# Performance work log

Measured on AMD Instinct MI355X. Metric: run time of the kernel, lower is better.

Reference implementation:

```python
import jax, jax.numpy as jnp
import numpy as np

B, L, H, NH = 4, 1024, 768, 12
NE, M, P = 30, 6, 600
EMB, BS, NC = 768, 16, 97
NEG = -1e30


def setup_inputs() -> dict:
    key = jax.random.key(0)
    ks = jax.random.split(key, 9)
    sequence_output = jax.random.normal(ks[0], (B, L, H), jnp.float32)
    attention = jax.random.uniform(ks[1], (B, NH, L, L), jnp.float32)
    mention_idx = jax.random.randint(ks[2], (B, NE, M), 0, L)
    mention_mask = jnp.ones((B, NE, M), jnp.float32)
    hts = jax.random.randint(ks[3], (B, P, 2), 0, NE)
    s = 0.02
    head_W = jax.random.normal(ks[4], (EMB, 2 * H), jnp.float32) * s
    head_b = jnp.zeros((EMB,), jnp.float32)
    tail_W = jax.random.normal(ks[5], (EMB, 2 * H), jnp.float32) * s
    tail_b = jnp.zeros((EMB,), jnp.float32)
    proj_W = jax.random.normal(ks[6], (H, EMB * BS), jnp.float32) * s
    cls_W = jax.random.normal(ks[7], (NC, H), jnp.float32) * s
    cls_b = jnp.zeros((NC,), jnp.float32)
    return {
        'sequence_output': sequence_output, 'attention': attention,
        'head_W': head_W, 'head_b': head_b, 'tail_W': tail_W, 'tail_b': tail_b,
        'proj_W': proj_W, 'cls_W': cls_W, 'cls_b': cls_b,
        'mention_mask': mention_mask, 'mention_idx': mention_idx, 'hts': hts,
    }


def reference(sequence_output, attention, head_W, head_b, tail_W, tail_b,
              proj_W, cls_W, cls_b, mention_mask, mention_idx, hts):
    b_, l_, h_ = sequence_output.shape
    bidx = jnp.arange(b_)[:, None, None]                     # [B,1,1]
    # ---- per-entity pooling (segment reduce over ragged mentions) ----
    m_emb = sequence_output[bidx, mention_idx]               # [B,NE,M,H]
    att_t = attention.transpose(0, 2, 1, 3)                  # [B,L,NH,L]
    m_att = att_t[bidx, mention_idx]                         # [B,NE,M,NH,L]
    masked = jnp.where(mention_mask[..., None] > 0, m_emb, NEG)
    e_emb = jax.nn.logsumexp(masked, axis=2)                 # [B,NE,H]
    cnt = jnp.maximum(mention_mask.sum(2), 1.0)              # [B,NE]
    e_att = (m_att * mention_mask[..., None, None]).sum(2) / cnt[..., None, None]  # [B,NE,NH,L]
    # ---- head/tail gathers over pairs ----
    b2 = jnp.arange(b_)[:, None]                             # [B,1]
    h_emb = e_emb[b2, hts[..., 0]]                           # [B,P,H]
    t_emb = e_emb[b2, hts[..., 1]]
    h_att = e_att[b2, hts[..., 0]]                           # [B,P,NH,L]
    t_att = e_att[b2, hts[..., 1]]
    ht_att = (h_att * t_att).mean(2)                         # [B,P,L]
    ht_att = ht_att / (ht_att.sum(-1, keepdims=True) + 1e-30)
    rs = jnp.einsum('bpl,blh->bph', ht_att, sequence_output) # [B,P,H]
    # ---- extractors + block-bilinear classifier ----
    hs = jnp.tanh(jnp.concatenate([h_emb, rs], -1) @ head_W.T + head_b)  # [B,P,EMB]
    ts = jnp.tanh(jnp.concatenate([t_emb, rs], -1) @ tail_W.T + tail_b)
    emb = hs.shape[-1]
    bs = proj_W.shape[1] // emb
    p_ = hs.shape[1]
    b1 = hs.reshape(b_, p_, emb // bs, bs)
    b2t = ts.reshape(b_, p_, emb // bs, bs)
    bl = (b1[..., :, None] * b2t[..., None, :]).reshape(b_, p_, emb * bs)
    logits = (bl @ proj_W.T) @ cls_W.T + cls_b               # [B,P,NC]
    return logits
```

## Files before the change

kernel.cpp:

```cpp
#include <hip/hip_runtime.h>
#include <cmath>

#define B_   4
#define L_   1024
#define H_   768
#define NH_  12
#define NE_  30
#define M_   6
#define P_   600
#define EMB_ 768
#define BS_  16
#define NC_  97

typedef __bf16 bf16x8 __attribute__((ext_vector_type(8)));
typedef float floatx4 __attribute__((ext_vector_type(4)));

union V16 { uint4 q; __bf16 b[8]; bf16x8 v; };
union V8  { unsigned long long u; __bf16 b[4]; };

__device__ __forceinline__ void gload16(const __bf16* g, __bf16* l) {
  __builtin_amdgcn_global_load_lds(
      (const __attribute__((address_space(1))) void*)g,
      (__attribute__((address_space(3))) void*)l, 16, 0, 0);
}

__device__ __forceinline__ void mfma_step(
    const __bf16* As, const __bf16* Bs,
    int ar, int bc, int frow, int kg, floatx4 acc[2][2])
{
  V16 a0, a1, b0, b1;
  a0.q = *reinterpret_cast<const uint4*>(As + (ar + frow) * 32 + kg * 8);
  a1.q = *reinterpret_cast<const uint4*>(As + (ar + 16 + frow) * 32 + kg * 8);
  b0.q = *reinterpret_cast<const uint4*>(Bs + (bc + frow) * 32 + kg * 8);
  b1.q = *reinterpret_cast<const uint4*>(Bs + (bc + 16 + frow) * 32 + kg * 8);
  acc[0][0] = __builtin_amdgcn_mfma_f32_16x16x32_bf16(a0.v, b0.v, acc[0][0], 0, 0, 0);
  acc[0][1] = __builtin_amdgcn_mfma_f32_16x16x32_bf16(a0.v, b1.v, acc[0][1], 0, 0, 0);
  acc[1][0] = __builtin_amdgcn_mfma_f32_16x16x32_bf16(a1.v, b0.v, acc[1][0], 0, 0, 0);
  acc[1][1] = __builtin_amdgcn_mfma_f32_16x16x32_bf16(a1.v, b1.v, acc[1][1], 0, 0, 0);
}

__device__ __forceinline__ void gemm_core(
    const __bf16* __restrict__ A, int lda, long aRow0,
    const __bf16* __restrict__ Bt, int ldb, long bRow0,
    int K, __bf16* sm, floatx4 acc[2][2])
{
  const int tid = threadIdx.x;
  const int lid = tid & 63, w = tid >> 6;
  const int ar = (w & 1) * 32, bc = (w >> 1) * 32;
  const int frow = lid & 15, kg = lid >> 4;
  const int grow = tid >> 2, gq = (tid & 3) * 8;
  const __bf16* ag = A + (aRow0 + grow) * (long)lda + gq;
  const __bf16* bg = Bt + (bRow0 + grow) * (long)ldb + gq;
  __bf16* wA = sm + w * 512;
  const int nt = K >> 5;
  gload16(ag, wA);
  gload16(bg, wA + 2048);
  gload16(ag + 32, wA + 4096);
  gload16(bg + 32, wA + 4096 + 2048);
  int cur = 0;
  for (int i = 0; i < nt - 1; ++i) {
    asm volatile("s_waitcnt vmcnt(2)" ::: "memory");
    __builtin_amdgcn_s_barrier();
    __builtin_amdgcn_sched_barrier(0);
    if (i + 2 < nt) {
      int nb = cur + 2; if (nb >= 3) nb -= 3;
      __bf16* d = sm + nb * 4096 + w * 512;
      gload16(ag + (i + 2) * 32, d);
      gload16(bg + (i + 2) * 32, d + 2048);
    }
    const __bf16* As = sm + cur * 4096;
    mfma_step(As, As + 2048, ar, bc, frow, kg, acc);
    cur += 1; if (cur == 3) cur = 0;
  }
  asm volatile("s_waitcnt vmcnt(0)" ::: "memory");
  __builtin_amdgcn_s_barrier();
  __builtin_amdgcn_sched_barrier(0);
  const __bf16* As = sm + cur * 4096;
  mfma_step(As, As + 2048, ar, bc, frow, kg, acc);
}

#define S1_CVT  2400
#define S1_TPW  9216
#define S1_TPS  3072
#define S1_POOL 120
#define S1_ATT  1440

__device__ __forceinline__ void transpose_body(
    const float* __restrict__ in, __bf16* __restrict__ out,
    int R, int C, int bx, int by, float (*t)[33])
{
  int c0 = bx*32, r0 = by*32;
  int tx = threadIdx.x & 31, ty = threadIdx.x >> 5;
#pragma unroll
  for (int p = 0; p < 4; ++p)
    t[ty + p*8][tx] = in[(long)(r0 + ty + p*8)*C + c0 + tx];
  __syncthreads();
#pragma unroll
  for (int p = 0; p < 4; ++p)
    out[(long)(c0 + ty + p*8)*R + r0 + tx] = (__bf16)t[tx][ty + p*8];
}

__global__ __launch_bounds__(256) void k_prep(
    const float* __restrict__ seq, const float* __restrict__ att,
    const float* __restrict__ headW, const float* __restrict__ tailW,
    const float* __restrict__ projW, const float* __restrict__ clsW,
    const float* __restrict__ mmask, const int* __restrict__ midx,
    __bf16* __restrict__ Wt, __bf16* __restrict__ clsA,
    __bf16* __restrict__ projWT, __bf16* __restrict__ seqT,
    __bf16* __restrict__ e_embB, __bf16* __restrict__ e_att)
{
  __shared__ float t[32][33];
  int blk = blockIdx.x;
  int tid = threadIdx.x;
  if (blk < S1_CVT) {
    int gid = blk*256 + tid;
    if (gid < 2*H_*384) {
      int sel = gid / (H_*384);
      int rem = gid % (H_*384);
      int o = rem / 384;
      int k4 = (rem % 384) * 4;
      const float* W = sel ? tailW : headW;
      float4 v = *reinterpret_cast<const float4*>(W + (long)o*(2*H_) + k4);
      V8 d; d.b[0]=(__bf16)v.x; d.b[1]=(__bf16)v.y; d.b[2]=(__bf16)v.z; d.b[3]=(__bf16)v.w;
      *reinterpret_cast<unsigned long long*>(Wt + ((long)sel*H_ + o)*(2*H_) + k4) = d.u;
    } else {
      int rem = gid - 2*H_*384;
      int row = rem / 192;
      int k4 = (rem % 192) * 4;
      V8 d;
      if (row < NC_) {
        float4 v = *reinterpret_cast<const float4*>(clsW + (long)row*H_ + k4);
        d.b[0]=(__bf16)v.x; d.b[1]=(__bf16)v.y; d.b[2]=(__bf16)v.z; d.b[3]=(__bf16)v.w;
      } else {
        d.b[0]=d.b[1]=d.b[2]=d.b[3]=(__bf16)0.f;
      }
      *reinterpret_cast<unsigned long long*>(clsA + (long)row*H_ + k4) = d.u;
    }
  } else if (blk < S1_CVT + S1_TPW) {
    int b = blk - S1_CVT;
    transpose_body(projW, projWT, H_, EMB_*BS_, b % 384, b / 384, t);
  } else if (blk < S1_CVT + S1_TPW + S1_TPS) {
    int b = blk - (S1_CVT + S1_TPW);
    int bx = b % 24, by = (b / 24) % 32, bz = b / (24*32);
    transpose_body(seq + (long)bz*L_*H_, seqT + (long)bz*H_*L_, L_, H_, bx, by, t);
  } else if (blk < S1_CVT + S1_TPW + S1_TPS + S1_POOL) {
    int be = blk - (S1_CVT + S1_TPW + S1_TPS);
    int idx[M_]; float msk[M_];
#pragma unroll
    for (int m = 0; m < M_; ++m) {
      idx[m] = midx[be * M_ + m];
      msk[m] = mmask[be * M_ + m];
    }
    int b = be / NE_;
    const float* sb = seq + (size_t)b * L_ * H_;
    for (int h = tid; h < H_; h += 256) {
      float v[M_]; float mx = -3.0e38f;
#pragma unroll
      for (int m = 0; m < M_; ++m) {
        float x = (msk[m] > 0.f) ? sb[(size_t)idx[m] * H_ + h] : -1e30f;
        v[m] = x; mx = fmaxf(mx, x);
      }
      float s = 0.f;
#pragma unroll
      for (int m = 0; m < M_; ++m) s += expf(v[m] - mx);
      e_embB[(size_t)be * H_ + h] = (__bf16)(mx + logf(s));
    }
  } else {
    int i = (blk - (S1_CVT + S1_TPW + S1_TPS + S1_POOL))*256 + tid;
    int l4 = (i & 255) * 4;
    int nh = (i >> 8) % NH_;
    int be = i / (256 * NH_);
    int b  = be / NE_;
    float s0=0.f, s1=0.f, s2=0.f, s3=0.f, cnt=0.f;
#pragma unroll
    for (int m = 0; m < M_; ++m) {
      float mk = mmask[be*M_ + m];
      cnt += mk;
      int id = midx[be*M_ + m];
      float4 a = *reinterpret_cast<const float4*>(
          att + (((size_t)b*NH_ + nh)*L_ + id)*L_ + l4);
      s0 += mk*a.x; s1 += mk*a.y; s2 += mk*a.z; s3 += mk*a.w;
    }
    float inv = 1.f / fmaxf(cnt, 1.f);
    V8 o;
    o.b[0]=(__bf16)(s0*inv); o.b[1]=(__bf16)(s1*inv);
    o.b[2]=(__bf16)(s2*inv); o.b[3]=(__bf16)(s3*inv);
    *reinterpret_cast<unsigned long long*>(e_att + ((size_t)be*NH_ + nh)*L_ + l4) = o.u;
  }
}

#define S2_WC  384
#define S2_PRE 48
#define S2_HT  2400

__global__ __launch_bounds__(256) void k_mid(
    const __bf16* __restrict__ clsA, const __bf16* __restrict__ projWT,
    const __bf16* __restrict__ e_att, const int* __restrict__ hts,
    const __bf16* __restrict__ e_embB, const __bf16* __restrict__ Wt,
    __bf16* __restrict__ WcT, __bf16* __restrict__ htatt,
    float* __restrict__ hpre, float* __restrict__ tpre)
{
  __shared__ __bf16 sm[3*4096];
  int blk = blockIdx.x;
  int tid = threadIdx.x;
  if (blk < S2_WC) {
    int n0 = (blk % 192)*64, r0 = (blk / 192)*64;
    floatx4 acc[2][2] = {};
    gemm_core(clsA, H_, r0, projWT, H_, n0, H_, sm, acc);
    int lid = tid & 63, w = tid >> 6;
    int ar = (w&1)*32, bc = (w>>1)*32, frow = lid&15, kg = lid>>4;
#pragma unroll
    for (int i = 0; i < 2; ++i)
#pragma unroll
      for (int r = 0; r < 4; ++r) {
        int c = r0 + ar + i*16 + kg*4 + r;
#pragma unroll
        for (int j = 0; j < 2; ++j)
          WcT[(long)c*(EMB_*BS_) + n0 + bc + j*16 + frow] = (__bf16)acc[i][j][r];
      }
  } else if (blk < S2_WC + S2_PRE) {
    int tb = blk - S2_WC;
    int o0 = (tb % 12)*64;
    int r0 = ((tb / 12) & 1)*64;
    int sel = tb / 24;
    floatx4 acc[2][2] = {};
    gemm_core(e_embB, H_, r0, Wt + (long)sel*H_*(2*H_), 2*H_, o0, H_, sm, acc);
    float* out = sel ? tpre : hpre;
    int lid = tid & 63, w = tid >> 6;
    int ar = (w&1)*32, bc = (w>>1)*32, frow = lid&15, kg = lid>>4;
#pragma unroll
    for (int i = 0; i < 2; ++i)
#pragma unroll
      for (int r = 0; r < 4; ++r) {
        int be = r0 + ar + i*16 + kg*4 + r;
        if (be < B_*NE_) {
#pragma unroll
          for (int j = 0; j < 2; ++j)
            out[(long)be*EMB_ + o0 + bc + j*16 + frow] = acc[i][j][r];
        }
      }
  } else {
    int bp = blk - (S2_WC + S2_PRE);
    int b = bp / P_;
    int hi = hts[bp*2 + 0], ti = hts[bp*2 + 1];
    const __bf16* ha = e_att + (size_t)(b*NE_ + hi) * NH_ * L_;
    const __bf16* ta = e_att + (size_t)(b*NE_ + ti) * NH_ * L_;
    int l4 = tid * 4;
    float v[4] = {0.f,0.f,0.f,0.f};
#pragma unroll
    for (int nh = 0; nh < NH_; ++nh) {
      V8 x, y;
      x.u = *reinterpret_cast<const unsigned long long*>(ha + nh*L_ + l4);
      y.u = *reinterpret_cast<const unsigned long long*>(ta + nh*L_ + l4);
#pragma unroll
      for (int q = 0; q < 4; ++q) v[q] += (float)x.b[q] * (float)y.b[q];
    }
    float loc = 0.f;
#pragma unroll
    for (int q = 0; q < 4; ++q) { v[q] *= (1.f/NH_); loc += v[q]; }
    float* red = reinterpret_cast<float*>(sm);
    for (int off = 32; off > 0; off >>= 1) loc += __shfl_down(loc, off, 64);
    if ((tid & 63) == 0) red[tid >> 6] = loc;
    __syncthreads();
    float inv = 1.f / (red[0] + red[1] + red[2] + red[3] + 1e-30f);
    V8 o;
#pragma unroll
    for (int q = 0; q < 4; ++q) o.b[q] = (__bf16)(v[q] * inv);
    *reinterpret_cast<unsigned long long*>(htatt + (size_t)bp*L_ + l4) = o.u;
  }
}

__global__ __launch_bounds__(256) void k_rs_mfma(
    const __bf16* __restrict__ htatt, const __bf16* __restrict__ seqT,
    __bf16* __restrict__ rs)
{
  __shared__ __bf16 sm[3*4096];
  int b = blockIdx.z, p0 = blockIdx.y*64, h0 = blockIdx.x*64;
  floatx4 acc[2][2] = {};
  gemm_core(htatt, L_, (long)b*P_ + p0, seqT + (long)b*H_*L_, L_, h0, L_, sm, acc);
  int lid = threadIdx.x & 63, w = threadIdx.x >> 6;
  int ar = (w&1)*32, bc = (w>>1)*32, frow = lid&15, kg = lid>>4;
#pragma unroll
  for (int i = 0; i < 2; ++i)
#pragma unroll
    for (int r = 0; r < 4; ++r) {
      int p = p0 + ar + i*16 + kg*4 + r;
      if (p < P_) {
#pragma unroll
        for (int j = 0; j < 2; ++j)
          rs[((long)b*P_ + p)*H_ + h0 + bc + j*16 + frow] = (__bf16)acc[i][j][r];
      }
    }
}

__global__ __launch_bounds__(256) void k_extract_mfma(
    const __bf16* __restrict__ rs, const __bf16* __restrict__ Wt,
    const float* __restrict__ headb, const float* __restrict__ tailb,
    const float* __restrict__ hpre, const float* __restrict__ tpre,
    const int* __restrict__ hts, __bf16* __restrict__ hs, __bf16* __restrict__ ts)
{
  __shared__ __bf16 sm[3*4096];
  int sel = blockIdx.z, r0 = blockIdx.y*64, o0 = blockIdx.x*64;
  const float* bias = sel ? tailb : headb;
  const float* pre = sel ? tpre : hpre;
  __bf16* out = sel ? ts : hs;
  floatx4 acc[2][2] = {};
  gemm_core(rs, H_, r0, Wt + (long)sel*H_*(2*H_) + H_, 2*H_, o0, H_, sm, acc);
  int lid = threadIdx.x & 63, w = threadIdx.x >> 6;
  int ar = (w&1)*32, bc = (w>>1)*32, frow = lid&15, kg = lid>>4;
#pragma unroll
  for (int i = 0; i < 2; ++i)
#pragma unroll
    for (int r = 0; r < 4; ++r) {
      int row = r0 + ar + i*16 + kg*4 + r;
      if (row < B_*P_) {
        int b = row / P_;
        int e = hts[row*2 + sel];
        const float* prow = pre + (long)(b*NE_ + e) * EMB_;
#pragma unroll
        for (int j = 0; j < 2; ++j) {
          int o = o0 + bc + j*16 + frow;
          out[(long)row*EMB_ + o] = (__bf16)tanhf(acc[i][j][r] + prow[o] + bias[o]);
        }
      }
    }
}

__global__ __launch_bounds__(512) void k_logits_mfma(
    const __bf16* __restrict__ hs, const __bf16* __restrict__ ts,
    const __bf16* __restrict__ WcT, const float* __restrict__ clsb,
    float* __restrict__ out)
{
  int r0 = (blockIdx.x >> 2) * 16;
  int ks = blockIdx.x & 3;
  int tid = threadIdx.x;
  int w = tid >> 6, lid = tid & 63;
  int frow = lid & 15, kg = lid >> 4;
  int row = r0 + frow;
  long hsrow = (long)row * EMB_;
  floatx4 acc[7] = {};
  int kbase0 = ks*3072 + w*384;
  for (int s = 0; s < 12; ++s) {
    int kb = kbase0 + s*32 + kg*8;
    int q16 = (kb >> 8) << 4;
    int ii = (kb >> 4) & 15;
    int jj0 = kb & 15;
    float hv = (float)hs[hsrow + q16 + ii];
    V16 tsv; tsv.q = *reinterpret_cast<const uint4*>(ts + hsrow + q16 + jj0);
    bf16x8 af;
#pragma unroll
    for (int j = 0; j < 8; ++j) af[j] = (__bf16)(hv * (float)tsv.b[j]);
#pragma unroll
    for (int f = 0; f < 7; ++f) {
      V16 bv; bv.q = *reinterpret_cast<const uint4*>(WcT + (long)(f*16 + frow)*(EMB_*BS_) + kb);
      acc[f] = __builtin_amdgcn_mfma_f32_16x16x32_bf16(af, bv.v, acc[f], 0, 0, 0);
    }
  }
  __shared__ float red[4][16][112];
#pragma unroll
  for (int f = 0; f < 7; ++f)
#pragma unroll
    for (int r = 0; r < 4; ++r) {
      if (w < 4) red[w][kg*4 + r][f*16 + frow] = acc[f][r];
    }
  __syncthreads();
#pragma unroll
  for (int f = 0; f < 7; ++f)
#pragma unroll
    for (int r = 0; r < 4; ++r) {
      if (w >= 4) red[w-4][kg*4 + r][f*16 + frow] += acc[f][r];
    }
  __syncthreads();
  for (int e = tid; e < 16*112; e += 512) {
    int rr = e / 112, cc = e % 112;
    if (cc < NC_) {
      float s = (ks == 0) ? clsb[cc] : 0.f;
#pragma unroll
      for (int ww = 0; ww < 4; ++ww) s += red[ww][rr][cc];
      atomicAdd(out + (long)(r0 + rr)*NC_ + cc, s);
    }
  }
}

extern "C" void kernel_launch(void* const* d_in, const int* in_sizes, int n_in,
                              void* d_out, int out_size, void* d_ws, size_t ws_size,
                              hipStream_t stream) {
  const float* seq   = (const float*)d_in[0];
  const float* att   = (const float*)d_in[1];
  const float* headW = (const float*)d_in[2];
  const float* headb = (const float*)d_in[3];
  const float* tailW = (const float*)d_in[4];
  const float* tailb = (const float*)d_in[5];
  const float* projW = (const float*)d_in[6];
  const float* clsW  = (const float*)d_in[7];
  const float* clsb  = (const float*)d_in[8];
  const float* mmask = (const float*)d_in[9];
  const int* midx = (const int*)d_in[10];
  const int* hts  = (const int*)d_in[11];

  char* p = (char*)d_ws;
  auto alloc_f = [&](size_t n){ float* r = (float*)p; p += n*sizeof(float); return r; };
  auto alloc_b = [&](size_t n){ __bf16* r = (__bf16*)p; p += n*2; return r; };
  float* hpre    = alloc_f((size_t)B_*NE_*EMB_);
  float* tpre    = alloc_f((size_t)B_*NE_*EMB_);
  __bf16* e_embB = alloc_b((size_t)128*H_);
  __bf16* e_att  = alloc_b((size_t)B_*NE_*NH_*L_);
  __bf16* htattb = alloc_b((size_t)2464*L_);
  __bf16* seqT   = alloc_b((size_t)B_*H_*L_);
  __bf16* rsb    = alloc_b((size_t)2432*H_);
  __bf16* Wt     = alloc_b((size_t)2*H_*2*H_);
  __bf16* clsA   = alloc_b((size_t)128*H_);
  __bf16* WcT    = alloc_b((size_t)128*EMB_*BS_);
  __bf16* projWT = alloc_b((size_t)EMB_*BS_*H_);
  __bf16* hsb = projWT;
  __bf16* tsb = projWT + (size_t)B_*P_*EMB_;

  hipMemsetAsync(d_out, 0, (size_t)B_*P_*NC_*sizeof(float), stream);

  k_prep<<<S1_CVT + S1_TPW + S1_TPS + S1_POOL + S1_ATT, 256, 0, stream>>>(
      seq, att, headW, tailW, projW, clsW, mmask, midx,
      Wt, clsA, projWT, seqT, e_embB, e_att);
  k_mid<<<S2_WC + S2_PRE + S2_HT, 256, 0, stream>>>(
      clsA, projWT, e_att, hts, e_embB, Wt, WcT, htattb, hpre, tpre);
  k_rs_mfma<<<dim3(H_/64, 10, B_), 256, 0, stream>>>(htattb, seqT, rsb);
  k_extract_mfma<<<dim3(EMB_/64, 38, 2), 256, 0, stream>>>(
      rsb, Wt, headb, tailb, hpre, tpre, hts, hsb, tsb);
  k_logits_mfma<<<600, 512, 0, stream>>>(hsb, tsb, WcT, clsb, (float*)d_out);
}
```

Baseline: 420.4 us.

## Use 64x64 vectorized transposes and restructure logits kernel tiling

The prep transposes move from 32x32 tiles with scalar loads to 64x64 tiles with float4 loads and 8-byte bf16 stores. The branch order in the prep kernel is also changed so that the gather-heavy attention and pooling blocks are scheduled first. The logits kernel now gives each block 64 rows across 4 wave row-groups and 8 K-splits, where each wave pair splits K in half, in place of 16 rows and 4 K-splits. This is meant to cut grid overhead and reuse the WcT loads across rows, at the cost of a larger shared transpose tile that lowers occupancy and a bounds check on the last partial row tile.

New measurement: 450.1 us. +7.1%, slower.

```diff
diff --git a/kernel.cpp b/kernel.cpp
--- a/kernel.cpp
+++ b/kernel.cpp
@@ -79,25 +79,36 @@
   mfma_step(As, As + 2048, ar, bc, frow, kg, acc);
 }
 
+#define S1_ATT  1440
+#define S1_POOL 120
+#define S1_TPS  768
+#define S1_TPW  2304
 #define S1_CVT  2400
-#define S1_TPW  9216
-#define S1_TPS  3072
-#define S1_POOL 120
-#define S1_ATT  1440
-
-__device__ __forceinline__ void transpose_body(
+
+__device__ __forceinline__ void transpose64(
     const float* __restrict__ in, __bf16* __restrict__ out,
-    int R, int C, int bx, int by, float (*t)[33])
-{
-  int c0 = bx*32, r0 = by*32;
-  int tx = threadIdx.x & 31, ty = threadIdx.x >> 5;
-#pragma unroll
-  for (int p = 0; p < 4; ++p)
-    t[ty + p*8][tx] = in[(long)(r0 + ty + p*8)*C + c0 + tx];
+    int R, int C, int bx, int by, float (*t)[65])
+{
+  int c0 = bx*64, r0 = by*64;
+  int tx = threadIdx.x & 15, ty = threadIdx.x >> 4;
+#pragma unroll
+  for (int p = 0; p < 4; ++p) {
+    float4 v = *reinterpret_cast<const float4*>(
+        in + (long)(r0 + ty + p*16)*C + c0 + tx*4);
+    t[ty + p*16][tx*4 + 0] = v.x;
+    t[ty + p*16][tx*4 + 1] = v.y;
+    t[ty + p*16][tx*4 + 2] = v.z;
+    t[ty + p*16][tx*4 + 3] = v.w;
+  }
   __syncthreads();
 #pragma unroll
-  for (int p = 0; p < 4; ++p)
-    out[(long)(c0 + ty + p*8)*R + r0 + tx] = (__bf16)t[tx][ty + p*8];
+  for (int p = 0; p < 4; ++p) {
+    V8 o;
+#pragma unroll
+    for (int i = 0; i < 4; ++i) o.b[i] = (__bf16)t[tx*4 + i][ty + p*16];
+    *reinterpret_cast<unsigned long long*>(
+        out + (long)(c0 + ty + p*16)*R + r0 + tx*4) = o.u;
+  }
 }
 
 __global__ __launch_bounds__(256) void k_prep(
@@ -109,11 +120,61 @@
     __bf16* __restrict__ projWT, __bf16* __restrict__ seqT,
     __bf16* __restrict__ e_embB, __bf16* __restrict__ e_att)
 {
-  __shared__ float t[32][33];
+  __shared__ float t[64][65];
   int blk = blockIdx.x;
   int tid = threadIdx.x;
-  if (blk < S1_CVT) {
-    int gid = blk*256 + tid;
+  if (blk < S1_ATT) {
+    int i = blk*256 + tid;
+    int l4 = (i & 255) * 4;
+    int nh = (i >> 8) % NH_;
+    int be = i / (256 * NH_);
+    int b  = be / NE_;
+    float s0=0.f, s1=0.f, s2=0.f, s3=0.f, cnt=0.f;
+#pragma unroll
+    for (int m = 0; m < M_; ++m) {
+      float mk = mmask[be*M_ + m];
+      cnt += mk;
+      int id = midx[be*M_ + m];
+      float4 a = *reinterpret_cast<const float4*>(
+          att + (((size_t)b*NH_ + nh)*L_ + id)*L_ + l4);
+      s0 += mk*a.x; s1 += mk*a.y; s2 += mk*a.z; s3 += mk*a.w;
+    }
+    float inv = 1.f / fmaxf(cnt, 1.f);
+    V8 o;
+    o.b[0]=(__bf16)(s0*inv); o.b[1]=(__bf16)(s1*inv);
+    o.b[2]=(__bf16)(s2*inv); o.b[3]=(__bf16)(s3*inv);
+    *reinterpret_cast<unsigned long long*>(e_att + ((size_t)be*NH_ + nh)*L_ + l4) = o.u;
+  } else if (blk < S1_ATT + S1_POOL) {
+    int be = blk - S1_ATT;
+    int idx[M_]; float msk[M_];
+#pragma unroll
+    for (int m = 0; m < M_; ++m) {
+      idx[m] = midx[be * M_ + m];
+      msk[m] = mmask[be * M_ + m];
+    }
+    int b = be / NE_;
+    const float* sb = seq + (size_t)b * L_ * H_;
+    for (int h = tid; h < H_; h += 256) {
+      float v[M_]; float mx = -3.0e38f;
+#pragma unroll
+      for (int m = 0; m < M_; ++m) {
+        float x = (msk[m] > 0.f) ? sb[(size_t)idx[m] * H_ + h] : -1e30f;
+        v[m] = x; mx = fmaxf(mx, x);
+      }
+      float s = 0.f;
+#pragma unroll
+      for (int m = 0; m < M_; ++m) s += expf(v[m] - mx);
+      e_embB[(size_t)be * H_ + h] = (__bf16)(mx + logf(s));
+    }
+  } else if (blk < S1_ATT + S1_POOL + S1_TPS) {
+    int b = blk - (S1_ATT + S1_POOL);
+    int bx = b % 12, by = (b / 12) % 16, bz = b / 192;
+    transpose64(seq + (long)bz*L_*H_, seqT + (long)bz*H_*L_, L_, H_, bx, by, t);
+  } else if (blk < S1_ATT + S1_POOL + S1_TPS + S1_TPW) {
+    int b = blk - (S1_ATT + S1_POOL + S1_TPS);
+    transpose64(projW, projWT, H_, EMB_*BS_, b % 192, b / 192, t);
+  } else {
+    int gid = (blk - (S1_ATT + S1_POOL + S1_TPS + S1_TPW))*256 + tid;
     if (gid < 2*H_*384) {
       int sel = gid / (H_*384);
       int rem = gid % (H_*384);
@@ -136,56 +197,6 @@
       }
       *reinterpret_cast<unsigned long long*>(clsA + (long)row*H_ + k4) = d.u;
     }
-  } else if (blk < S1_CVT + S1_TPW) {
-    int b = blk - S1_CVT;
-    transpose_body(projW, projWT, H_, EMB_*BS_, b % 384, b / 384, t);
-  } else if (blk < S1_CVT + S1_TPW + S1_TPS) {
-    int b = blk - (S1_CVT + S1_TPW);
-    int bx = b % 24, by = (b / 24) % 32, bz = b / (24*32);
-    transpose_body(seq + (long)bz*L_*H_, seqT + (long)bz*H_*L_, L_, H_, bx, by, t);
-  } else if (blk < S1_CVT + S1_TPW + S1_TPS + S1_POOL) {
-    int be = blk - (S1_CVT + S1_TPW + S1_TPS);
-    int idx[M_]; float msk[M_];
-#pragma unroll
-    for (int m = 0; m < M_; ++m) {
-      idx[m] = midx[be * M_ + m];
-      msk[m] = mmask[be * M_ + m];
-    }
-    int b = be / NE_;
-    const float* sb = seq + (size_t)b * L_ * H_;
-    for (int h = tid; h < H_; h += 256) {
-      float v[M_]; float mx = -3.0e38f;
-#pragma unroll
-      for (int m = 0; m < M_; ++m) {
-        float x = (msk[m] > 0.f) ? sb[(size_t)idx[m] * H_ + h] : -1e30f;
-        v[m] = x; mx = fmaxf(mx, x);
-      }
-      float s = 0.f;
-#pragma unroll
-      for (int m = 0; m < M_; ++m) s += expf(v[m] - mx);
-      e_embB[(size_t)be * H_ + h] = (__bf16)(mx + logf(s));
-    }
-  } else {
-    int i = (blk - (S1_CVT + S1_TPW + S1_TPS + S1_POOL))*256 + tid;
-    int l4 = (i & 255) * 4;
-    int nh = (i >> 8) % NH_;
-    int be = i / (256 * NH_);
-    int b  = be / NE_;
-    float s0=0.f, s1=0.f, s2=0.f, s3=0.f, cnt=0.f;
-#pragma unroll
-    for (int m = 0; m < M_; ++m) {
-      float mk = mmask[be*M_ + m];
-      cnt += mk;
-      int id = midx[be*M_ + m];
-      float4 a = *reinterpret_cast<const float4*>(
-          att + (((size_t)b*NH_ + nh)*L_ + id)*L_ + l4);
-      s0 += mk*a.x; s1 += mk*a.y; s2 += mk*a.z; s3 += mk*a.w;
-    }
-    float inv = 1.f / fmaxf(cnt, 1.f);
-    V8 o;
-    o.b[0]=(__bf16)(s0*inv); o.b[1]=(__bf16)(s1*inv);
-    o.b[2]=(__bf16)(s2*inv); o.b[3]=(__bf16)(s3*inv);
-    *reinterpret_cast<unsigned long long*>(e_att + ((size_t)be*NH_ + nh)*L_ + l4) = o.u;
   }
 }
 
@@ -331,16 +342,17 @@
     const __bf16* __restrict__ WcT, const float* __restrict__ clsb,
     float* __restrict__ out)
 {
-  int r0 = (blockIdx.x >> 2) * 16;
-  int ks = blockIdx.x & 3;
+  int rt = blockIdx.x >> 3;
+  int ks = blockIdx.x & 7;
   int tid = threadIdx.x;
   int w = tid >> 6, lid = tid & 63;
+  int rg = w & 3, kh = w >> 2;
   int frow = lid & 15, kg = lid >> 4;
-  int row = r0 + frow;
+  int row = rt*64 + rg*16 + frow;
   long hsrow = (long)row * EMB_;
   floatx4 acc[7] = {};
-  int kbase0 = ks*3072 + w*384;
-  for (int s = 0; s < 12; ++s) {
+  int kbase0 = ks*1536 + kh*768;
+  for (int s = 0; s < 24; ++s) {
     int kb = kbase0 + s*32 + kg*8;
     int q16 = (kb >> 8) << 4;
     int ii = (kb >> 4) & 15;
@@ -357,27 +369,28 @@
     }
   }
   __shared__ float red[4][16][112];
-#pragma unroll
-  for (int f = 0; f < 7; ++f)
-#pragma unroll
-    for (int r = 0; r < 4; ++r) {
-      if (w < 4) red[w][kg*4 + r][f*16 + frow] = acc[f][r];
-    }
+  if (kh == 0) {
+#pragma unroll
+    for (int f = 0; f < 7; ++f)
+#pragma unroll
+      for (int r = 0; r < 4; ++r)
+        red[rg][kg*4 + r][f*16 + frow] = acc[f][r];
+  }
   __syncthreads();
-#pragma unroll
-  for (int f = 0; f < 7; ++f)
-#pragma unroll
-    for (int r = 0; r < 4; ++r) {
-      if (w >= 4) red[w-4][kg*4 + r][f*16 + frow] += acc[f][r];
-    }
+  if (kh == 1) {
+#pragma unroll
+    for (int f = 0; f < 7; ++f)
+#pragma unroll
+      for (int r = 0; r < 4; ++r)
+        red[rg][kg*4 + r][f*16 + frow] += acc[f][r];
+  }
   __syncthreads();
-  for (int e = tid; e < 16*112; e += 512) {
+  for (int e = tid; e < 64*112; e += 512) {
     int rr = e / 112, cc = e % 112;
-    if (cc < NC_) {
-      float s = (ks == 0) ? clsb[cc] : 0.f;
-#pragma unroll
-      for (int ww = 0; ww < 4; ++ww) s += red[ww][rr][cc];
-      atomicAdd(out + (long)(r0 + rr)*NC_ + cc, s);
+    int ro = rt*64 + rr;
+    if (cc < NC_ && ro < B_*P_) {
+      float s = red[rr >> 4][rr & 15][cc] + ((ks == 0) ? clsb[cc] : 0.f);
+      atomicAdd(out + (long)ro*NC_ + cc, s);
     }
   }
 }
@@ -417,7 +430,7 @@
 
   hipMemsetAsync(d_out, 0, (size_t)B_*P_*NC_*sizeof(float), stream);
 
-  k_prep<<<S1_CVT + S1_TPW + S1_TPS + S1_POOL + S1_ATT, 256, 0, stream>>>(
+  k_prep<<<S1_ATT + S1_POOL + S1_TPS + S1_TPW + S1_CVT, 256, 0, stream>>>(
       seq, att, headW, tailW, projW, clsW, mmask, midx,
       Wt, clsA, projWT, seqT, e_embB, e_att);
   k_mid<<<S2_WC + S2_PRE + S2_HT, 256, 0, stream>>>(
@@ -425,5 +438,5 @@
   k_rs_mfma<<<dim3(H_/64, 10, B_), 256, 0, stream>>>(htattb, seqT, rsb);
   k_extract_mfma<<<dim3(EMB_/64, 38, 2), 256, 0, stream>>>(
       rsb, Wt, headb, tailb, hpre, tpre, hts, hsb, tsb);
-  k_logits_mfma<<<600, 512, 0, stream>>>(hsb, tsb, WcT, clsb, (float*)d_out);
-}
+  k_logits_mfma<<<304, 512, 0, stream>>>(hsb, tsb, WcT, clsb, (float*)d_out);
+}
```
